# Kernel optimization log

Hardware: AMD Instinct MI355X
Metric: run time of the kernel (lower is better)

Reference implementation:

```python
import jax, jax.numpy as jnp
import numpy as np

PATCH = 3  # patch_size=3, stride=1
B, C, H, W = 8, 256, 64, 64


def _extract_patches(x):
    # x: (c, h, w) -> (c*PATCH*PATCH, N) with N = (h-2)*(w-2), valid 3x3 patches
    c, h, w = x.shape
    hh, ww = h - PATCH + 1, w - PATCH + 1
    pats = jnp.stack([x[:, i:i + hh, j:j + ww]
                      for i in range(PATCH) for j in range(PATCH)], axis=0)  # (9, c, hh, ww)
    return pats.reshape(PATCH * PATCH * c, hh * ww)


def _index_to_flow(max_idx):
    # max_idx: (hh, ww) int -> flow (h, w, 2) padded by 2 at bottom/right
    hh, ww = max_idx.shape
    flow_w = (max_idx % ww).astype(jnp.float32)
    flow_h = (max_idx // ww).astype(jnp.float32)
    gy, gx = jnp.meshgrid(jnp.arange(hh, dtype=jnp.float32),
                          jnp.arange(ww, dtype=jnp.float32), indexing='ij')
    flow = jnp.stack((flow_w - gx, flow_h - gy), axis=2)  # (hh, ww, 2)
    return jnp.pad(flow, ((0, 2), (0, 2), (0, 0)))


def _per_image(feat_in, feat_ref):
    c, h, w = feat_in.shape
    hh, ww = h - PATCH + 1, w - PATCH + 1
    # channel-wise L2 normalize each spatial position (F.normalize dim=0, eps=1e-12)
    feat_in = feat_in / jnp.maximum(jnp.linalg.norm(feat_in, axis=0, keepdims=True), 1e-12)
    feat_ref = feat_ref / jnp.maximum(jnp.linalg.norm(feat_ref, axis=0, keepdims=True), 1e-12)
    Pi = _extract_patches(feat_in)    # (k, N)
    Pr = _extract_patches(feat_ref)   # (k, N)
    # is_norm=True: normalize ref patches (norm + 1e-5, per BasicSR feature_match_index)
    Pr = Pr / (jnp.linalg.norm(Pr, axis=0, keepdims=True) + 1e-5)
    corr = Pi.T @ Pr                  # (N, N) exhaustive patch correlation
    max_val = corr.max(axis=1)
    max_idx = jnp.argmax(corr, axis=1)
    # norm_input=True: divide by input patch norms
    max_val = max_val / jnp.linalg.norm(Pi, axis=0)
    max_val = max_val.reshape(hh, ww)
    max_idx = max_idx.reshape(hh, ww)
    sim = jnp.pad(max_val, ((1, 1), (1, 1)))[None]  # (1, h, w)
    flow = _index_to_flow(max_idx)                   # (h, w, 2)
    # nine down-right shifts (fill 0 at top-left), tensor_shift semantics
    shifted = jnp.stack([jnp.pad(flow[:h - i, :w - j], ((i, 0), (j, 0), (0, 0)))
                         for i in range(3) for j in range(3)], axis=0)  # (9, h, w, 2)
    return flow, shifted, sim


def setup_inputs() -> dict:
    key = jax.random.key(0)
    k1, k2 = jax.random.split(key)
    features1 = jax.random.normal(k1, (B, C, H, W), dtype=jnp.float32)
    features2 = jax.random.normal(k2, (B, C, H, W), dtype=jnp.float32)
    return {"features1": features1, "features2": features2}


def reference(features1, features2):
    pre_flow, pre_offset, pre_similarity = jax.vmap(_per_image)(features1, features2)
    # pre_flow: (b,h,w,2); pre_offset: (b,9,h,w,2); pre_similarity: (b,1,h,w)
    return pre_flow, pre_offset, pre_similarity
```

## Files before the change

kernel.cpp:

```cpp
#include <hip/hip_runtime.h>

typedef unsigned short u16;
typedef unsigned char u8;
typedef unsigned int u32;
typedef __bf16 bf16x8 __attribute__((ext_vector_type(8)));
typedef float f32x4 __attribute__((ext_vector_type(4)));

constexpr int BATCH = 8;
constexpr int C = 256;
constexpr int H = 64;
constexpr int W = 64;
constexpr int HW = H * W;
constexpr int HH = 62, WW = 62;
constexpr int NQ = HH * WW;
constexpr int SEG = 8;
constexpr int NBLK_RED = 536;

constexpr size_t OFF_RNORM = 0;
constexpr size_t OFF_RESV = 262144;
constexpr size_t OFF_RESI = 385280;
constexpr size_t OFF_SLOT0 = 508416;
constexpr size_t SP_H1 = 0;
constexpr size_t SP_L1 = 2097152;
constexpr size_t SP_H2 = 4194304;
constexpr size_t SP_L2 = 6291456;
constexpr size_t SP_P = 8388608;
constexpr size_t SP_PIDX8 = 75497472;
constexpr size_t SLOT_BYTES = 77594624;

typedef const __attribute__((address_space(1))) unsigned int* gas_ptr;
typedef __attribute__((address_space(3))) unsigned int* las_ptr;
__device__ __forceinline__ void gl16(const void* g, void* l) {
  __builtin_amdgcn_global_load_lds((gas_ptr)g, (las_ptr)l, 16, 0, 0);
}

__device__ __forceinline__ int pre_of(int ki) {
  if (ki <= 62) return ki * (ki + 1) / 2;
  int r = 123 - ki;
  return 1953 + 1891 - r * (r + 1) / 2;
}

__global__ __launch_bounds__(256) void norm_kernel(const float* __restrict__ f1,
                                                   const float* __restrict__ f2,
                                                   float* __restrict__ rnorm) {
  int by = blockIdx.x;
  int tensor = blockIdx.y;
  const float* f = tensor ? f2 : f1;
  int b = by >> 6, y = by & 63;
  int x = threadIdx.x & 63;
  int cq = threadIdx.x >> 6;
  const float* base = f + ((size_t)b * C) * HW + y * W + x;
  float s = 0.f;
  for (int c = cq; c < C; c += 4) {
    float v = base[(size_t)c * HW];
    s = fmaf(v, v, s);
  }
  __shared__ float sm[4][64];
  sm[cq][x] = s;
  __syncthreads();
  if (threadIdx.x < 64) {
    float t = sm[0][x] + sm[1][x] + sm[2][x] + sm[3][x];
    float nrm = fmaxf(sqrtf(t), 1e-12f);
    rnorm[((size_t)tensor * BATCH + b) * HW + y * W + x] = 1.0f / nrm;
  }
}

__global__ __launch_bounds__(256) void convert_kernel(const float* __restrict__ f1,
                                                      const float* __restrict__ f2,
                                                      const float* __restrict__ rnorm,
                                                      int bi,
                                                      u16* __restrict__ hi1, u16* __restrict__ lo1,
                                                      u16* __restrict__ hi2, u16* __restrict__ lo2) {
  int chunk = blockIdx.x;
  int tensor = blockIdx.y;
  int pos0 = chunk * 32;
  const float* f = (tensor ? f2 : f1) + (size_t)bi * C * HW;
  const float* rn = rnorm + ((size_t)tensor * BATCH + bi) * HW + pos0;
  u16* dh = (tensor ? hi2 : hi1) + (size_t)pos0 * C;
  u16* dl = (tensor ? lo2 : lo1) + (size_t)pos0 * C;

  __shared__ u32 sm[32][257];
  int t = threadIdx.x;
  int px = t & 31, cg = t >> 5;
  float r = rn[px];
  for (int kk = 0; kk < 32; ++kk) {
    int c = (cg << 5) + kk;
    float v = f[(size_t)c * HW + pos0 + px] * r;
    __bf16 h = (__bf16)v;
    float hf = (float)h;
    __bf16 lo = (__bf16)(v - hf);
    sm[px][c] = ((u32)__builtin_bit_cast(u16, h) << 16) | (u32)__builtin_bit_cast(u16, lo);
  }
  __syncthreads();
  int px2 = t >> 3, seg = t & 7;
  int c0 = seg * 32;
  for (int g8 = 0; g8 < 4; ++g8) {
    u32 hw0, hw1, hw2, hw3, lw0, lw1, lw2, lw3;
    u32 a, b2;
    a = sm[px2][c0 + g8 * 8 + 0]; b2 = sm[px2][c0 + g8 * 8 + 1];
    hw0 = (a >> 16) | (b2 & 0xFFFF0000u); lw0 = (a & 0xFFFFu) | (b2 << 16);
    a = sm[px2][c0 + g8 * 8 + 2]; b2 = sm[px2][c0 + g8 * 8 + 3];
    hw1 = (a >> 16) | (b2 & 0xFFFF0000u); lw1 = (a & 0xFFFFu) | (b2 << 16);
    a = sm[px2][c0 + g8 * 8 + 4]; b2 = sm[px2][c0 + g8 * 8 + 5];
    hw2 = (a >> 16) | (b2 & 0xFFFF0000u); lw2 = (a & 0xFFFFu) | (b2 << 16);
    a = sm[px2][c0 + g8 * 8 + 6]; b2 = sm[px2][c0 + g8 * 8 + 7];
    hw3 = (a >> 16) | (b2 & 0xFFFF0000u); lw3 = (a & 0xFFFFu) | (b2 << 16);
    size_t off = (size_t)px2 * C + c0 + g8 * 8;
    uint4 hv; hv.x = hw0; hv.y = hw1; hv.z = hw2; hv.w = hw3;
    uint4 lv; lv.x = lw0; lv.y = lw1; lv.z = lw2; lv.w = lw3;
    *(uint4*)(dh + off) = hv;
    *(uint4*)(dl + off) = lv;
  }
}

__global__ __launch_bounds__(256, 2) void pgemm_kernel(const u16* __restrict__ hi1,
                                                       const u16* __restrict__ lo1,
                                                       const u16* __restrict__ hi2,
                                                       const u16* __restrict__ lo2,
                                                       float* __restrict__ P) {
  int bid = blockIdx.x;
  int swz = (bid & 7) * 128 + (bid >> 3);
  int p0 = (swz >> 5) << 7, q0 = (swz & 31) << 7;

  __shared__ __align__(16) char smem[65536];
  char* sAh = smem;
  char* sAl = smem + 16384;
  char* sBh = smem + 32768;
  char* sBl = smem + 49152;

  int t = threadIdx.x;
  int l = t & 63, w = t >> 6, wm = w >> 1, wn = w & 1;
  int lr = l & 15, lh = l >> 4;
  int wv = w;

  const u16* src0 = hi1 + (size_t)p0 * 256;
  const u16* src1 = lo1 + (size_t)p0 * 256;
  const u16* src2 = hi2 + (size_t)q0 * 256;
  const u16* src3 = lo2 + (size_t)q0 * 256;

  f32x4 acc[4][4];
#pragma unroll
  for (int mf = 0; mf < 4; ++mf)
#pragma unroll
    for (int nf = 0; nf < 4; ++nf)
      acc[mf][nf] = (f32x4){0.f, 0.f, 0.f, 0.f};

  for (int kt = 0; kt < 4; ++kt) {
    if (kt) __syncthreads();
#pragma unroll
    for (int qq = 0; qq < 4; ++qq) {
      int q = wv * 4 + qq;
      int row = q * 8 + (l >> 3);
      int cc = l & 7;
      size_t goff = (size_t)row * 256 + kt * 64 + ((cc ^ (row & 7)) << 3);
      gl16(src0 + goff, sAh + q * 1024);
      gl16(src1 + goff, sAl + q * 1024);
      gl16(src2 + goff, sBh + q * 1024);
      gl16(src3 + goff, sBl + q * 1024);
    }
    __syncthreads();
#pragma unroll
    for (int ks = 0; ks < 2; ++ks) {
      bf16x8 ah[4], al[4];
#pragma unroll
      for (int mf = 0; mf < 4; ++mf) {
        int row = wm * 64 + mf * 16 + lr;
        int off = row * 128 + ((((ks * 4 + lh) << 4)) ^ ((row & 7) << 4));
        ah[mf] = *(const bf16x8*)(sAh + off);
        al[mf] = *(const bf16x8*)(sAl + off);
      }
#pragma unroll
      for (int nf = 0; nf < 4; ++nf) {
        int row = wn * 64 + nf * 16 + lr;
        int off = row * 128 + ((((ks * 4 + lh) << 4)) ^ ((row & 7) << 4));
        bf16x8 bh = *(const bf16x8*)(sBh + off);
        bf16x8 bl = *(const bf16x8*)(sBl + off);
#pragma unroll
        for (int mf = 0; mf < 4; ++mf) {
          acc[mf][nf] = __builtin_amdgcn_mfma_f32_16x16x32_bf16(ah[mf], bh, acc[mf][nf], 0, 0, 0);
          acc[mf][nf] = __builtin_amdgcn_mfma_f32_16x16x32_bf16(al[mf], bh, acc[mf][nf], 0, 0, 0);
          acc[mf][nf] = __builtin_amdgcn_mfma_f32_16x16x32_bf16(ah[mf], bl, acc[mf][nf], 0, 0, 0);
        }
      }
    }
  }

#pragma unroll
  for (int mf = 0; mf < 4; ++mf)
#pragma unroll
    for (int nf = 0; nf < 4; ++nf)
#pragma unroll
      for (int j = 0; j < 4; ++j) {
        int pg = p0 + wm * 64 + mf * 16 + lh * 4 + j;
        int qg = q0 + wn * 64 + nf * 16 + lr;
        size_t addr = (((size_t)((pg >> 6) << 6 | (qg >> 6))) << 12) +
                      ((pg & 63) << 6) + (qg & 63);
        P[addr] = acc[mf][nf][j];
      }
}

__global__ __launch_bounds__(512) void reduce_kernel(char* __restrict__ slot0,
                                                     size_t slotBytes) {
  int slot = blockIdx.y;
  char* sb = slot0 + (size_t)slot * slotBytes;
  const float* P = (const float*)(sb + SP_P);
  float* pval8 = (float*)sb;
  u8* pidx8 = (u8*)(sb + SP_PIDX8);

  int bid = blockIdx.x;
  int ki = 0;
  for (ki = 0; ki < 123; ++ki) {
    int d = ki - 61; if (d < 0) d = -d;
    int ns = (62 - d + SEG - 1) / SEG;
    if (bid < ns) break;
    bid -= ns;
  }
  int k = ki - 61;
  int ystart = k < 0 ? -k : 0;
  int yend = k > 0 ? 61 - k : 61;
  int y0 = ystart + bid * SEG;
  int y1 = y0 + SEG; if (y1 > yend + 1) y1 = yend + 1;
  int sid0 = pre_of(ki) + (y0 - ystart);

  __shared__ __align__(16) float LSLOT[2][4096];

  int t = threadIdx.x;
  int w = t >> 6, l = t & 63;

  auto issue = [&](int p) {
    const float* gp = P + ((size_t)((p << 6) + (p + k)) << 12);
#pragma unroll
    for (int qq = 0; qq < 2; ++qq) {
      int q = w * 2 + qq;
      int r = q * 4 + (l >> 4);
      int ccs = l & 15;
      const float* src = gp + r * 64 + ((ccs ^ (r & 15)) << 2);
      gl16(src, (char*)(&LSLOT[p & 1][0]) + q * 1024);
    }
  };

  auto presum = [&](int p, float* Dg) {
    const float* S = &LSLOT[p & 1][0];
    float A[12], B[12], Cc[12];
#pragma unroll
    for (int dx = 0; dx < 3; ++dx) {
      int row = l + dx; if (row > 63) row = 63;
      float* dst = dx == 0 ? A : (dx == 1 ? B : Cc);
#pragma unroll
      for (int j3 = 0; j3 < 3; ++j3) {
        int ch = (2 * w + j3) & 15;
        float4 v = *(const float4*)(S + row * 64 + ((ch ^ (row & 15)) << 2));
        dst[j3 * 4 + 0] = v.x; dst[j3 * 4 + 1] = v.y;
        dst[j3 * 4 + 2] = v.z; dst[j3 * 4 + 3] = v.w;
      }
    }
#pragma unroll
    for (int bb = 0; bb < 8; ++bb)
      Dg[bb] = A[bb] + B[bb + 1] + Cc[bb + 2];
  };

  auto candstep = [&](int y, const float* D0, const float* D1, const float* D2) {
    float best = __uint_as_float(0xFF800000u);
    int bbb = 0;
#pragma unroll
    for (int bb = 0; bb < 8; ++bb) {
      float c = D0[bb] + D1[bb] + D2[bb];
      bool valid = (w * 8 + bb) <= 61;
      if (valid && c > best) { best = c; bbb = bb; }
    }
    size_t o = (size_t)(sid0 + (y - y0)) * 512 + (w << 6) + l;
    pval8[o] = best;
    pidx8[o] = (u8)bbb;
  };

  float DgA[8], DgB[8], DgC[8];

  issue(y0);
  issue(y0 + 1);
  __syncthreads();
  presum(y0, DgA);
  __syncthreads();
  issue(y0 + 2);
  __syncthreads();
  presum(y0 + 1, DgB);

  int y = y0;
  while (true) {
    __syncthreads();
    if (y + 1 < y1) issue(y + 3);
    presum(y + 2, DgC);
    candstep(y, DgA, DgB, DgC);
    if (++y >= y1) break;
    __syncthreads();
    if (y + 1 < y1) issue(y + 3);
    presum(y + 2, DgA);
    candstep(y, DgB, DgC, DgA);
    if (++y >= y1) break;
    __syncthreads();
    if (y + 1 < y1) issue(y + 3);
    presum(y + 2, DgB);
    candstep(y, DgC, DgA, DgB);
    if (++y >= y1) break;
  }
}

__global__ __launch_bounds__(256) void combine_kernel(const char* __restrict__ slot0,
                                                      size_t slotBytes, int b0,
                                                      float* __restrict__ resv,
                                                      int* __restrict__ residx) {
  int q = blockIdx.x * 256 + threadIdx.x;
  if (q >= NQ) return;
  int slot = blockIdx.y;
  int b = b0 + slot;
  const char* sb = slot0 + (size_t)slot * slotBytes;
  const float* pval8 = (const float*)sb;
  const u8* pidx8 = (const u8*)(sb + SP_PIDX8);
  int y = q / 62, ax = q - y * 62;
  float best = __uint_as_float(0xFF800000u);
  int bjy = 0, bw = 0;
  for (int jy = 0; jy < 62; ++jy) {
    int ki = 61 + jy - y;
    int sid = pre_of(ki) + (y < jy ? y : jy);
    const float* p = pval8 + (size_t)sid * 512 + ax;
#pragma unroll
    for (int ww = 0; ww < 8; ++ww) {
      float v = p[ww << 6];
      if (v > best) { best = v; bjy = jy; bw = ww; }
    }
  }
  int kib = 61 + bjy - y;
  int sidb = pre_of(kib) + (y < bjy ? y : bjy);
  int bb = pidx8[(size_t)sidb * 512 + (bw << 6) + ax];
  resv[(size_t)b * NQ + q] = best;
  residx[(size_t)b * NQ + q] = bjy * 62 + bw * 8 + bb;
}

__global__ __launch_bounds__(256) void assemble_kernel(const float* __restrict__ res_val,
                                                       const int* __restrict__ res_idx,
                                                       float* __restrict__ out) {
  int gid = blockIdx.x * 256 + threadIdx.x;
  if (gid >= BATCH * HW) return;
  int b = gid >> 12;
  int y = (gid >> 6) & 63;
  int x = gid & 63;

  float* out_flow = out;
  float* out_off = out + (size_t)BATCH * HW * 2;
  float* out_sim = out + (size_t)BATCH * HW * 2 + (size_t)BATCH * 9 * HW * 2;

  auto flow_at = [&](int yy, int xx, float* fx, float* fy) {
    if (yy >= 0 && yy < HH && xx >= 0 && xx < WW) {
      int idx = res_idx[(size_t)b * NQ + yy * WW + xx];
      *fx = (float)(idx % WW - xx);
      *fy = (float)(idx / WW - yy);
    } else {
      *fx = 0.f;
      *fy = 0.f;
    }
  };

  float fx, fy;
  flow_at(y, x, &fx, &fy);
  size_t fo = ((size_t)b * HW + y * W + x) * 2;
  out_flow[fo + 0] = fx;
  out_flow[fo + 1] = fy;

#pragma unroll
  for (int sft = 0; sft < 9; ++sft) {
    int i = sft / 3, j = sft % 3;
    float ox, oy;
    flow_at(y - i, x - j, &ox, &oy);
    size_t o = (((size_t)b * 9 + sft) * HW + y * W + x) * 2;
    out_off[o + 0] = ox;
    out_off[o + 1] = oy;
  }

  float sim = 0.f;
  if (y >= 1 && y <= HH && x >= 1 && x <= WW) {
    float mv = res_val[(size_t)b * NQ + (y - 1) * WW + (x - 1)];
    sim = mv * (1.0f / ((3.0f + 1e-5f) * 3.0f));
  }
  out_sim[(size_t)b * HW + y * W + x] = sim;
}

extern "C" void kernel_launch(void* const* d_in, const int* in_sizes, int n_in,
                              void* d_out, int out_size, void* d_ws, size_t ws_size,
                              hipStream_t stream) {
  const float* f1 = (const float*)d_in[0];
  const float* f2 = (const float*)d_in[1];
  float* out = (float*)d_out;
  char* ws = (char*)d_ws;

  float* rnorm = (float*)(ws + OFF_RNORM);
  float* resv = (float*)(ws + OFF_RESV);
  int* residx = (int*)(ws + OFF_RESI);
  char* slot0 = ws + OFF_SLOT0;

  int nslots = 1;
  if (ws_size > OFF_SLOT0 + SLOT_BYTES) {
    size_t n = (ws_size - OFF_SLOT0) / SLOT_BYTES;
    nslots = n >= 8 ? 8 : (int)n;
    if (nslots < 1) nslots = 1;
  }

  norm_kernel<<<dim3(BATCH * H, 2), 256, 0, stream>>>(f1, f2, rnorm);

  for (int b0 = 0; b0 < BATCH; b0 += nslots) {
    int g = BATCH - b0 < nslots ? BATCH - b0 : nslots;
    for (int i = 0; i < g; ++i) {
      char* slot = slot0 + (size_t)i * SLOT_BYTES;
      convert_kernel<<<dim3(128, 2), 256, 0, stream>>>(
          f1, f2, rnorm, b0 + i,
          (u16*)(slot + SP_H1), (u16*)(slot + SP_L1),
          (u16*)(slot + SP_H2), (u16*)(slot + SP_L2));
      pgemm_kernel<<<1024, 256, 0, stream>>>(
          (const u16*)(slot + SP_H1), (const u16*)(slot + SP_L1),
          (const u16*)(slot + SP_H2), (const u16*)(slot + SP_L2),
          (float*)(slot + SP_P));
    }
    reduce_kernel<<<dim3(NBLK_RED, g), 512, 0, stream>>>(slot0, SLOT_BYTES);
    combine_kernel<<<dim3(16, g), 256, 0, stream>>>(slot0, SLOT_BYTES, b0,
                                                    resv, residx);
  }

  int total = BATCH * HW;
  assemble_kernel<<<(total + 255) / 256, 256, 0, stream>>>(resv, residx, out);
}
```

Baseline: 561.8 us.

## Fuse horizontal 3-tap presum into GEMM epilogue and simplify reduce kernel

The GEMM epilogue now stages each 64x64 accumulator tile through shared memory, computes the horizontal 3-tap diagonal partial sums there, and writes them transposed to global memory. The reduce kernel no longer needs LDS staging, swizzled async loads or barriers. It reads the presummed values directly with coalesced loads into a register pipeline and only does the vertical 3-tap sum plus the argmax. This moves work into the GEMM and removes synchronisation from the reduce, at the cost of extra LDS passes and barriers in the GEMM epilogue and more strided transposed global stores.

```diff
diff --git a/kernel.cpp b/kernel.cpp
--- a/kernel.cpp
+++ b/kernel.cpp
@@ -185,25 +185,55 @@
     }
   }
 
-#pragma unroll
-  for (int mf = 0; mf < 4; ++mf)
-#pragma unroll
-    for (int nf = 0; nf < 4; ++nf)
-#pragma unroll
-      for (int j = 0; j < 4; ++j) {
-        int pg = p0 + wm * 64 + mf * 16 + lh * 4 + j;
-        int qg = q0 + wn * 64 + nf * 16 + lr;
-        size_t addr = (((size_t)((pg >> 6) << 6 | (qg >> 6))) << 12) +
-                      ((pg & 63) << 6) + (qg & 63);
-        P[addr] = acc[mf][nf][j];
-      }
+  __syncthreads();
+  float* sq = (float*)smem;
+#pragma unroll
+  for (int pass = 0; pass < 2; ++pass) {
+    if (pass) __syncthreads();
+    if (wn == pass) {
+      float* buf = sq + wm * 4352;
+#pragma unroll
+      for (int mf = 0; mf < 4; ++mf)
+#pragma unroll
+        for (int nf = 0; nf < 4; ++nf)
+#pragma unroll
+          for (int j = 0; j < 4; ++j)
+            buf[(mf * 16 + lh * 4 + j) * 68 + nf * 16 + lr] = acc[mf][nf][j];
+      buf[l * 68 + 64] = 0.f;
+      buf[l * 68 + 65] = 0.f;
+    }
+    __syncthreads();
+    int sel = t >> 7, r = (t >> 1) & 63, half = t & 1;
+    const float* S = sq + sel * 4352;
+    int r1 = r + 1 > 63 ? 63 : r + 1;
+    int r2 = r + 2 > 63 ? 63 : r + 2;
+    const float* S0 = S + r * 68;
+    const float* S1 = S + r1 * 68;
+    const float* S2 = S + r2 * 68;
+    int planeIdx = (((p0 >> 6) + sel) << 6) + (q0 >> 6) + pass;
+    float* Qg = P + (((size_t)planeIdx) << 12) + r;
+#pragma unroll
+    for (int gi = 0; gi < 8; ++gi) {
+      int g = half * 8 + gi;
+      f32x4 a = *(const f32x4*)(S0 + g * 4);
+      f32x4 b0 = *(const f32x4*)(S1 + g * 4);
+      f32x4 c0 = *(const f32x4*)(S2 + g * 4);
+      float b4 = S1[g * 4 + 4];
+      float c4 = S2[g * 4 + 4];
+      float c5 = S2[g * 4 + 5];
+      Qg[(size_t)(g * 4 + 0) * 64] = a[0] + b0[1] + c0[2];
+      Qg[(size_t)(g * 4 + 1) * 64] = a[1] + b0[2] + c0[3];
+      Qg[(size_t)(g * 4 + 2) * 64] = a[2] + b0[3] + c4;
+      Qg[(size_t)(g * 4 + 3) * 64] = a[3] + b4 + c5;
+    }
+  }
 }
 
 __global__ __launch_bounds__(512) void reduce_kernel(char* __restrict__ slot0,
                                                      size_t slotBytes) {
   int slot = blockIdx.y;
   char* sb = slot0 + (size_t)slot * slotBytes;
-  const float* P = (const float*)(sb + SP_P);
+  const float* QT = (const float*)(sb + SP_P);
   float* pval8 = (float*)sb;
   u8* pidx8 = (u8*)(sb + SP_PIDX8);
 
@@ -221,86 +251,56 @@
   int y0 = ystart + bid * SEG;
   int y1 = y0 + SEG; if (y1 > yend + 1) y1 = yend + 1;
   int sid0 = pre_of(ki) + (y0 - ystart);
-
-  __shared__ __align__(16) float LSLOT[2][4096];
+  int pmax = yend + 2;
 
   int t = threadIdx.x;
   int w = t >> 6, l = t & 63;
 
-  auto issue = [&](int p) {
-    const float* gp = P + ((size_t)((p << 6) + (p + k)) << 12);
-#pragma unroll
-    for (int qq = 0; qq < 2; ++qq) {
-      int q = w * 2 + qq;
-      int r = q * 4 + (l >> 4);
-      int ccs = l & 15;
-      const float* src = gp + r * 64 + ((ccs ^ (r & 15)) << 2);
-      gl16(src, (char*)(&LSLOT[p & 1][0]) + q * 1024);
-    }
-  };
-
-  auto presum = [&](int p, float* Dg) {
-    const float* S = &LSLOT[p & 1][0];
-    float A[12], B[12], Cc[12];
-#pragma unroll
-    for (int dx = 0; dx < 3; ++dx) {
-      int row = l + dx; if (row > 63) row = 63;
-      float* dst = dx == 0 ? A : (dx == 1 ? B : Cc);
-#pragma unroll
-      for (int j3 = 0; j3 < 3; ++j3) {
-        int ch = (2 * w + j3) & 15;
-        float4 v = *(const float4*)(S + row * 64 + ((ch ^ (row & 15)) << 2));
-        dst[j3 * 4 + 0] = v.x; dst[j3 * 4 + 1] = v.y;
-        dst[j3 * 4 + 2] = v.z; dst[j3 * 4 + 3] = v.w;
-      }
-    }
-#pragma unroll
-    for (int bb = 0; bb < 8; ++bb)
-      Dg[bb] = A[bb] + B[bb + 1] + Cc[bb + 2];
+  float A[8], B[8], P0[8], P1[8], P2[8];
+
+  auto ld = [&](int p, float* D) {
+    const float* gp = QT + (((size_t)((p << 6) + (p + k))) << 12) + (w << 9) + l;
+#pragma unroll
+    for (int s = 0; s < 8; ++s) D[s] = gp[s << 6];
   };
 
   auto candstep = [&](int y, const float* D0, const float* D1, const float* D2) {
     float best = __uint_as_float(0xFF800000u);
     int bbb = 0;
 #pragma unroll
-    for (int bb = 0; bb < 8; ++bb) {
-      float c = D0[bb] + D1[bb] + D2[bb];
-      bool valid = (w * 8 + bb) <= 61;
-      if (valid && c > best) { best = c; bbb = bb; }
+    for (int s = 0; s < 8; ++s) {
+      float c = D0[s] + D1[s] + D2[s];
+      bool valid = (w * 8 + s) <= 61;
+      if (valid && c > best) { best = c; bbb = s; }
     }
     size_t o = (size_t)(sid0 + (y - y0)) * 512 + (w << 6) + l;
     pval8[o] = best;
     pidx8[o] = (u8)bbb;
   };
 
-  float DgA[8], DgB[8], DgC[8];
-
-  issue(y0);
-  issue(y0 + 1);
-  __syncthreads();
-  presum(y0, DgA);
-  __syncthreads();
-  issue(y0 + 2);
-  __syncthreads();
-  presum(y0 + 1, DgB);
+  ld(y0, A);
+  ld(y0 + 1, B);
+  ld(y0 + 2, P0);
+  ld(y0 + 3 > pmax ? pmax : y0 + 3, P1);
+  ld(y0 + 4 > pmax ? pmax : y0 + 4, P2);
 
   int y = y0;
   while (true) {
-    __syncthreads();
-    if (y + 1 < y1) issue(y + 3);
-    presum(y + 2, DgC);
-    candstep(y, DgA, DgB, DgC);
+    candstep(y, A, B, P0);
+#pragma unroll
+    for (int s = 0; s < 8; ++s) { A[s] = B[s]; B[s] = P0[s]; }
     if (++y >= y1) break;
-    __syncthreads();
-    if (y + 1 < y1) issue(y + 3);
-    presum(y + 2, DgA);
-    candstep(y, DgB, DgC, DgA);
+    ld(y + 4 > pmax ? pmax : y + 4, P0);
+    candstep(y, A, B, P1);
+#pragma unroll
+    for (int s = 0; s < 8; ++s) { A[s] = B[s]; B[s] = P1[s]; }
     if (++y >= y1) break;
-    __syncthreads();
-    if (y + 1 < y1) issue(y + 3);
-    presum(y + 2, DgB);
-    candstep(y, DgC, DgA, DgB);
+    ld(y + 4 > pmax ? pmax : y + 4, P1);
+    candstep(y, A, B, P2);
+#pragma unroll
+    for (int s = 0; s < 8; ++s) { A[s] = B[s]; B[s] = P2[s]; }
     if (++y >= y1) break;
+    ld(y + 4 > pmax ? pmax : y + 4, P2);
   }
 }
 
```

Result: slower. 590.7 us (+5.1%).
